# Kernel tuning notes

Hardware: AMD Instinct MI355X
Metric: run time of the kernel (lower is better)

Reference implementation:

```python
import jax, jax.numpy as jnp
import numpy as np

B, N, DIM, H = 512, 98, 512, 16
HD = DIM // H
WS = (2, 7, 7)  # window size; N == 2*7*7


def _relative_position_index(ws):
    d, h, w = ws
    coords = np.stack(np.meshgrid(np.arange(d), np.arange(h), np.arange(w), indexing='ij'))
    cf = coords.reshape(3, -1)  # [3, N]
    rel = cf[:, :, None] - cf[:, None, :]  # [3, N, N]
    rel = rel.transpose(1, 2, 0).astype(np.int64)
    rel[:, :, 0] += d - 1
    rel[:, :, 1] += h - 1
    rel[:, :, 2] += w - 1
    rel[:, :, 0] *= (2 * h - 1) * (2 * w - 1)
    rel[:, :, 1] *= 2 * w - 1
    return rel.sum(-1)  # [N, N] in [0, (2d-1)(2h-1)(2w-1))


def setup_inputs() -> dict:
    key = jax.random.key(0)
    ks = jax.random.split(key, 6)
    table_size = (2 * WS[0] - 1) * (2 * WS[1] - 1) * (2 * WS[2] - 1)  # 507
    return {
        'x': jax.random.normal(ks[0], (B, N, DIM), jnp.float32),
        'qkv_w': jax.random.normal(ks[1], (DIM, 3 * DIM), jnp.float32) * 0.02,
        'qkv_b': jnp.zeros((3 * DIM,), jnp.float32),
        'proj_w': jax.random.normal(ks[2], (DIM, DIM), jnp.float32) * 0.02,
        'proj_b': jnp.zeros((DIM,), jnp.float32),
        'bias_table': jax.random.normal(ks[3], (table_size, H), jnp.float32) * 0.02,
        'rel_index': jnp.asarray(_relative_position_index(WS)),
    }


def reference(x, qkv_w, qkv_b, proj_w, proj_b, bias_table, rel_index):
    b, n, c = x.shape
    scale = HD ** -0.5
    qkv = (x @ qkv_w + qkv_b).reshape(b, n, 3, H, HD)
    qkv = jnp.transpose(qkv, (2, 0, 3, 1, 4))  # [3, B, H, N, HD]
    q, k, v = qkv[0] * scale, qkv[1], qkv[2]
    attn = jnp.einsum('bhnd,bhmd->bhnm', q, k)  # [B, H, N, N]
    # gather relative position bias: [N,N] indices into [table, H] -> [H, N, N]
    bias = jnp.transpose(bias_table[rel_index], (2, 0, 1))
    attn = jax.nn.softmax(attn + bias[None], axis=-1)
    out = jnp.einsum('bhnm,bhmd->bhnd', attn, v)  # [B, H, N, HD]
    out = jnp.transpose(out, (0, 2, 1, 3)).reshape(b, n, c)
    return out @ proj_w + proj_b
```

## Files before the change

kernel.cpp:

```cpp
#include <hip/hip_runtime.h>

typedef unsigned short u16;
typedef __bf16 bf16x8 __attribute__((ext_vector_type(8)));
typedef float f32x4 __attribute__((ext_vector_type(4)));

typedef __attribute__((address_space(1))) const void* as1_cvp;
typedef __attribute__((address_space(3))) void* as3_vp;

__device__ __forceinline__ float b2f(u16 u) {
  union { unsigned int i; float f; } x; x.i = ((unsigned int)u) << 16; return x.f;
}
__device__ __forceinline__ u16 f2b(float f) {
  union { float f; unsigned int i; } x; x.f = f;
  unsigned int u = x.i;
  u += 0x7fffu + ((u >> 16) & 1u);
  return (u16)(u >> 16);
}

__global__ void k_detect(const u16* __restrict__ x, int* __restrict__ flag) {
  int t = threadIdx.x;
  int sane = 0;
#pragma unroll
  for (int i = 0; i < 8; ++i) {
    u16 u = x[t * 8 + i];
    int e = (u >> 7) & 0xFF;
    sane += (u == 0 || (e >= 100 && e <= 150)) ? 1 : 0;
  }
#pragma unroll
  for (int off = 32; off >= 1; off >>= 1) sane += __shfl_xor(sane, off);
  if (t == 0) *flag = (sane < 480) ? 1 : 0;
}

__global__ void k_convert(const void* __restrict__ xin, u16* __restrict__ xb,
                          const int* __restrict__ flagp) {
  if (!*flagp) return;
  long i = ((long)blockIdx.x * 256 + threadIdx.x) * 4;
  float4 v = *(const float4*)((const float*)xin + i);
  u16* o = xb + i;
  o[0] = f2b(v.x); o[1] = f2b(v.y); o[2] = f2b(v.z); o[3] = f2b(v.w);
}

__global__ void k_transpose(const void* __restrict__ W, u16* __restrict__ WT,
                            const int* __restrict__ flagp, int K, int N) {
  __shared__ u16 tile[32][33];
  int f = *flagp;
  int n0 = blockIdx.x * 32, k0 = blockIdx.y * 32;
  int tx = threadIdx.x, ty = threadIdx.y;
#pragma unroll
  for (int i = 0; i < 32; i += 8) {
    long idx = (long)(k0 + ty + i) * N + n0 + tx;
    tile[ty + i][tx] = f ? f2b(((const float*)W)[idx]) : ((const u16*)W)[idx];
  }
  __syncthreads();
#pragma unroll
  for (int i = 0; i < 32; i += 8)
    WT[(long)(n0 + ty + i) * K + k0 + tx] = tile[tx][ty + i];
}

__global__ void k_biasfrag(const int* __restrict__ rel, const void* __restrict__ table,
                           u16* __restrict__ biasFrag, const int* __restrict__ flagp) {
  int t = blockIdx.x * 256 + threadIdx.x;
  int f = *flagp;
  int ln = t & 63, r2 = t >> 6;
  int tj = r2 & 7, r3 = r2 >> 3;
  int ti = r3 % 7, h = r3 / 7;
  int col = ln & 15, qrow = ln >> 4;
  int j = tj * 16 + col;
  u16 v[4];
#pragma unroll
  for (int r = 0; r < 4; ++r) {
    int i = ti * 16 + qrow * 4 + r; if (i > 97) i = 97;
    float val;
    if (j < 98) {
      int rr = rel[i * 98 + j];
      val = f ? ((const float*)table)[rr * 16 + h] : b2f(((const u16*)table)[rr * 16 + h]);
    } else {
      val = -1e30f;
    }
    v[r] = f2b(val);
  }
  ushort4 out; out.x = v[0]; out.y = v[1]; out.z = v[2]; out.w = v[3];
  *(ushort4*)(biasFrag + (long)t * 4) = out;
}

__global__ __launch_bounds__(256) void k_gemm_bt(
    const u16* __restrict__ A_raw, const u16* __restrict__ A_conv,
    const u16* __restrict__ BT, const void* __restrict__ bias, void* __restrict__ C,
    const int* __restrict__ flagp, int N, int K, int out_follows_flag) {
  __shared__ __align__(16) u16 As[128 * 32];
  __shared__ __align__(16) u16 Bs[128 * 32];
  const int f = *flagp;
  const u16* A = f ? A_conv : A_raw;
  const int t = threadIdx.x, w = t >> 6, ln = t & 63;
  const long bm = (long)blockIdx.x * 128, bn = (long)blockIdx.y * 128;
  const int lrow = ln >> 2, lseg = ln & 3;
  const u16* ag0 = A + (bm + w * 32 + lrow) * (long)K + lseg * 8;
  const u16* ag1 = ag0 + 16L * K;
  const u16* bg0 = BT + (bn + w * 32 + lrow) * (long)K + lseg * 8;
  const u16* bg1 = bg0 + 16L * K;
  u16* As0 = &As[w * 1024]; u16* As1 = &As[w * 1024 + 512];
  u16* Bs0 = &Bs[w * 1024]; u16* Bs1 = &Bs[w * 1024 + 512];
  const int wm = w & 1, wn = w >> 1;
  const int col = ln & 15, qrow = ln >> 4;
  f32x4 acc[4][4] = {};
  for (int k0 = 0; k0 < K; k0 += 32) {
    __syncthreads();
    __builtin_amdgcn_global_load_lds((as1_cvp)(const void*)(ag0 + k0), (as3_vp)As0, 16, 0, 0);
    __builtin_amdgcn_global_load_lds((as1_cvp)(const void*)(ag1 + k0), (as3_vp)As1, 16, 0, 0);
    __builtin_amdgcn_global_load_lds((as1_cvp)(const void*)(bg0 + k0), (as3_vp)Bs0, 16, 0, 0);
    __builtin_amdgcn_global_load_lds((as1_cvp)(const void*)(bg1 + k0), (as3_vp)Bs1, 16, 0, 0);
    __syncthreads();
    bf16x8 af[4], bfr[4];
#pragma unroll
    for (int mi = 0; mi < 4; ++mi)
      af[mi] = *(const bf16x8*)&As[(wm * 64 + mi * 16 + col) * 32 + qrow * 8];
#pragma unroll
    for (int ni = 0; ni < 4; ++ni)
      bfr[ni] = *(const bf16x8*)&Bs[(wn * 64 + ni * 16 + col) * 32 + qrow * 8];
#pragma unroll
    for (int mi = 0; mi < 4; ++mi)
#pragma unroll
      for (int ni = 0; ni < 4; ++ni)
        acc[mi][ni] = __builtin_amdgcn_mfma_f32_16x16x32_bf16(af[mi], bfr[ni], acc[mi][ni], 0, 0, 0);
  }
  const int of = out_follows_flag ? f : 0;
  float bv[4];
#pragma unroll
  for (int ni = 0; ni < 4; ++ni) {
    long c = bn + wn * 64 + ni * 16 + col;
    bv[ni] = f ? ((const float*)bias)[c] : b2f(((const u16*)bias)[c]);
  }
#pragma unroll
  for (int mi = 0; mi < 4; ++mi)
#pragma unroll
    for (int ni = 0; ni < 4; ++ni)
#pragma unroll
      for (int r = 0; r < 4; ++r) {
        long row = bm + wm * 64 + mi * 16 + qrow * 4 + r;
        long c = bn + wn * 64 + ni * 16 + col;
        float v = acc[mi][ni][r] + bv[ni];
        if (of) ((float*)C)[row * N + c] = v;
        else    ((u16*)C)[row * N + c] = f2b(v);
      }
}

__global__ __launch_bounds__(256) void k_attn(
    const u16* __restrict__ qkv, const u16* __restrict__ biasFrag,
    u16* __restrict__ attnout) {
  __shared__ __align__(16) u16 Qs[112 * 32];
  __shared__ __align__(16) u16 Ks[128 * 32];
  __shared__ __align__(16) u16 Vt[32 * 136];
  __shared__ __align__(16) u16 Ps[4][16 * 136];
  const int b = blockIdx.x, h = blockIdx.y;
  const int t = threadIdx.x, w = t >> 6, ln = t & 63;
  const u16* qbase = qkv + (long)b * 98 * 1536 + h * 32;
  {
    const int gr = ln >> 2, gc = (ln & 3) * 8;
    for (int n = w; n < 7; n += 4) {
      int g = n * 16 + gr; if (g > 97) g = 97;
      __builtin_amdgcn_global_load_lds((as1_cvp)(const void*)(qbase + (long)g * 1536 + gc),
                                       (as3_vp)(Qs + n * 512), 16, 0, 0);
    }
    for (int n = w; n < 8; n += 4) {
      int g = n * 16 + gr; if (g > 97) g = 97;
      __builtin_amdgcn_global_load_lds((as1_cvp)(const void*)(qbase + 512 + (long)g * 1536 + gc),
                                       (as3_vp)(Ks + n * 512), 16, 0, 0);
    }
  }
  for (int z = t; z < 32 * 19; z += 256) {
    int d = z / 19, q = z % 19;
    *(unsigned int*)&Vt[d * 136 + 98 + q * 2] = 0u;
  }
  for (int idx = t; idx < 784; idx += 256) {
    int i = idx >> 3, c4 = (idx & 7) * 4;
    ushort4 v4 = *(const ushort4*)(qbase + 1024 + (long)i * 1536 + c4);
    Vt[(c4 + 0) * 136 + i] = v4.x;
    Vt[(c4 + 1) * 136 + i] = v4.y;
    Vt[(c4 + 2) * 136 + i] = v4.z;
    Vt[(c4 + 3) * 136 + i] = v4.w;
  }
  __syncthreads();
  const int col = ln & 15, qrow = ln >> 4;
  const float scale = 0.17677669529663687f;
  u16* Psw = &Ps[w][0];
  f32x4 o[2][2] = {{{0.f,0.f,0.f,0.f},{0.f,0.f,0.f,0.f}},{{0.f,0.f,0.f,0.f},{0.f,0.f,0.f,0.f}}};
  for (int tt = 0; tt < 2; ++tt) {
    const int ti = w + tt * 4;
    if (ti >= 7) break;
    const u16* bp = biasFrag + ((long)((h * 7 + ti) * 8) * 64 + ln) * 4;
    ushort4 bfv[8];
#pragma unroll
    for (int tj = 0; tj < 8; ++tj) bfv[tj] = *(const ushort4*)(bp + tj * 256);
    bf16x8 aq = *(const bf16x8*)&Qs[(ti * 16 + col) * 32 + qrow * 8];
    f32x4 s[8];
#pragma unroll
    for (int tj = 0; tj < 8; ++tj) {
      bf16x8 bk = *(const bf16x8*)&Ks[(tj * 16 + col) * 32 + qrow * 8];
      f32x4 z = {0.f, 0.f, 0.f, 0.f};
      s[tj] = __builtin_amdgcn_mfma_f32_16x16x32_bf16(aq, bk, z, 0, 0, 0);
    }
#pragma unroll
    for (int r = 0; r < 4; ++r) {
      float vals[8]; float m = -1e30f;
#pragma unroll
      for (int tj = 0; tj < 8; ++tj) {
        u16 bb = (r == 0) ? bfv[tj].x : (r == 1) ? bfv[tj].y : (r == 2) ? bfv[tj].z : bfv[tj].w;
        float v = fmaf(s[tj][r], scale, b2f(bb));
        vals[tj] = v; m = fmaxf(m, v);
      }
#pragma unroll
      for (int off = 1; off < 16; off <<= 1) m = fmaxf(m, __shfl_xor(m, off));
      float sum = 0.f;
#pragma unroll
      for (int tj = 0; tj < 8; ++tj) { vals[tj] = __expf(vals[tj] - m); sum += vals[tj]; }
#pragma unroll
      for (int off = 1; off < 16; off <<= 1) sum += __shfl_xor(sum, off);
      float inv = 1.f / sum;
      const int rt = qrow * 4 + r;
#pragma unroll
      for (int tj = 0; tj < 8; ++tj)
        Psw[rt * 136 + tj * 16 + col] = f2b(vals[tj] * inv);
    }
#pragma unroll
    for (int ks = 0; ks < 4; ++ks) {
      bf16x8 ap  = *(const bf16x8*)&Psw[col * 136 + ks * 32 + qrow * 8];
      bf16x8 bv0 = *(const bf16x8*)&Vt[col * 136 + ks * 32 + qrow * 8];
      bf16x8 bv1 = *(const bf16x8*)&Vt[(16 + col) * 136 + ks * 32 + qrow * 8];
      o[tt][0] = __builtin_amdgcn_mfma_f32_16x16x32_bf16(ap, bv0, o[tt][0], 0, 0, 0);
      o[tt][1] = __builtin_amdgcn_mfma_f32_16x16x32_bf16(ap, bv1, o[tt][1], 0, 0, 0);
    }
  }
  __syncthreads();
  u16* Os = Qs;
#pragma unroll
  for (int tt = 0; tt < 2; ++tt) {
    const int ti = w + tt * 4;
    if (ti >= 7) continue;
#pragma unroll
    for (int r = 0; r < 4; ++r) {
      const int i = ti * 16 + qrow * 4 + r;
      if (i < 98) {
        Os[i * 32 + col]      = f2b(o[tt][0][r]);
        Os[i * 32 + 16 + col] = f2b(o[tt][1][r]);
      }
    }
  }
  __syncthreads();
  u16* obase = attnout + (long)b * 98 * 512 + h * 32;
  for (int idx = t; idx < 784; idx += 256) {
    int i = idx >> 3, c4 = (idx & 7) * 4;
    *(ushort4*)(obase + (long)i * 512 + c4) = *(const ushort4*)&Os[i * 32 + c4];
  }
}

extern "C" void kernel_launch(void* const* d_in, const int* in_sizes, int n_in,
                              void* d_out, int out_size, void* d_ws, size_t ws_size,
                              hipStream_t stream) {
  (void)in_sizes; (void)n_in; (void)out_size; (void)ws_size;
  char* p = (char*)d_ws;
  u16* qkvbuf   = (u16*)p;  p += 50176L * 1536 * 2;
  u16* attnbuf  = (u16*)p;  u16* xb = attnbuf; p += 50176L * 512 * 2;
  u16* wqkvT    = (u16*)p;  p += 1536L * 512 * 2;
  u16* wprojT   = (u16*)p;  p += 512L * 512 * 2;
  u16* biasFrag = (u16*)p;  p += 57344L * 4 * 2;
  int* flagp    = (int*)p;

  k_detect<<<1, 64, 0, stream>>>((const u16*)d_in[0], flagp);
  k_convert<<<25088, 256, 0, stream>>>(d_in[0], xb, flagp);
  k_transpose<<<dim3(48, 16), dim3(32, 8), 0, stream>>>(d_in[1], wqkvT, flagp, 512, 1536);
  k_transpose<<<dim3(16, 16), dim3(32, 8), 0, stream>>>(d_in[3], wprojT, flagp, 512, 512);
  k_biasfrag<<<224, 256, 0, stream>>>((const int*)d_in[6], d_in[5], biasFrag, flagp);
  k_gemm_bt<<<dim3(392, 12), 256, 0, stream>>>((const u16*)d_in[0], xb, wqkvT, d_in[2],
                                               qkvbuf, flagp, 1536, 512, 0);
  k_attn<<<dim3(512, 16), 256, 0, stream>>>(qkvbuf, biasFrag, attnbuf);
  k_gemm_bt<<<dim3(392, 4), 256, 0, stream>>>(attnbuf, attnbuf, wprojT, d_in[4],
                                              d_out, flagp, 512, 512, 1);
}
```

Baseline: 464.8 us.

## Write QKV in per-head contiguous layout, XCD-aware GEMM tile mapping, BK=64

New measurement: 504.2 us. 8.5% more time.

```diff
diff --git a/kernel.cpp b/kernel.cpp
--- a/kernel.cpp
+++ b/kernel.cpp
@@ -86,42 +86,54 @@
 __global__ __launch_bounds__(256) void k_gemm_bt(
     const u16* __restrict__ A_raw, const u16* __restrict__ A_conv,
     const u16* __restrict__ BT, const void* __restrict__ bias, void* __restrict__ C,
-    const int* __restrict__ flagp, int N, int K, int out_follows_flag) {
-  __shared__ __align__(16) u16 As[128 * 32];
-  __shared__ __align__(16) u16 Bs[128 * 32];
+    const int* __restrict__ flagp, int N, int K, int out_follows_flag,
+    int qkv_mode, int NT) {
+  __shared__ __align__(16) u16 As[128 * 64];
+  __shared__ __align__(16) u16 Bs[128 * 64];
   const int f = *flagp;
   const u16* A = f ? A_conv : A_raw;
   const int t = threadIdx.x, w = t >> 6, ln = t & 63;
-  const long bm = (long)blockIdx.x * 128, bn = (long)blockIdx.y * 128;
-  const int lrow = ln >> 2, lseg = ln & 3;
-  const u16* ag0 = A + (bm + w * 32 + lrow) * (long)K + lseg * 8;
-  const u16* ag1 = ag0 + 16L * K;
-  const u16* bg0 = BT + (bn + w * 32 + lrow) * (long)K + lseg * 8;
-  const u16* bg1 = bg0 + 16L * K;
-  u16* As0 = &As[w * 1024]; u16* As1 = &As[w * 1024 + 512];
-  u16* Bs0 = &Bs[w * 1024]; u16* Bs1 = &Bs[w * 1024 + 512];
+  const unsigned p = blockIdx.x, xcd = p & 7, q = p >> 3;
+  const unsigned qd = q / (unsigned)NT;
+  const unsigned mt = xcd * 49u + qd, nt = q - qd * (unsigned)NT;
+  const long bm = (long)mt * 128, bn = (long)nt * 128;
+  const int r16 = ln & 15, seg = ln >> 4;
+  const u16* agp[4]; const u16* bgp[4];
+#pragma unroll
+  for (int i = 0; i < 4; ++i) {
+    int c = w * 4 + i, rc = c >> 1, kh = c & 1;
+    agp[i] = A  + (bm + rc * 16 + r16) * (long)K + kh * 32 + seg * 8;
+    bgp[i] = BT + (bn + rc * 16 + r16) * (long)K + kh * 32 + seg * 8;
+  }
   const int wm = w & 1, wn = w >> 1;
   const int col = ln & 15, qrow = ln >> 4;
   f32x4 acc[4][4] = {};
-  for (int k0 = 0; k0 < K; k0 += 32) {
+  for (int k0 = 0; k0 < K; k0 += 64) {
     __syncthreads();
-    __builtin_amdgcn_global_load_lds((as1_cvp)(const void*)(ag0 + k0), (as3_vp)As0, 16, 0, 0);
-    __builtin_amdgcn_global_load_lds((as1_cvp)(const void*)(ag1 + k0), (as3_vp)As1, 16, 0, 0);
-    __builtin_amdgcn_global_load_lds((as1_cvp)(const void*)(bg0 + k0), (as3_vp)Bs0, 16, 0, 0);
-    __builtin_amdgcn_global_load_lds((as1_cvp)(const void*)(bg1 + k0), (as3_vp)Bs1, 16, 0, 0);
+#pragma unroll
+    for (int i = 0; i < 4; ++i) {
+      int c = w * 4 + i;
+      __builtin_amdgcn_global_load_lds((as1_cvp)(const void*)(agp[i] + k0),
+                                       (as3_vp)(As + c * 512), 16, 0, 0);
+      __builtin_amdgcn_global_load_lds((as1_cvp)(const void*)(bgp[i] + k0),
+                                       (as3_vp)(Bs + c * 512), 16, 0, 0);
+    }
     __syncthreads();
-    bf16x8 af[4], bfr[4];
-#pragma unroll
-    for (int mi = 0; mi < 4; ++mi)
-      af[mi] = *(const bf16x8*)&As[(wm * 64 + mi * 16 + col) * 32 + qrow * 8];
-#pragma unroll
-    for (int ni = 0; ni < 4; ++ni)
-      bfr[ni] = *(const bf16x8*)&Bs[(wn * 64 + ni * 16 + col) * 32 + qrow * 8];
-#pragma unroll
-    for (int mi = 0; mi < 4; ++mi)
+#pragma unroll
+    for (int kh = 0; kh < 2; ++kh) {
+      bf16x8 af[4], bfr[4];
+#pragma unroll
+      for (int mi = 0; mi < 4; ++mi)
+        af[mi] = *(const bf16x8*)&As[(((wm * 4 + mi) << 1) | kh) * 512 + qrow * 128 + col * 8];
 #pragma unroll
       for (int ni = 0; ni < 4; ++ni)
-        acc[mi][ni] = __builtin_amdgcn_mfma_f32_16x16x32_bf16(af[mi], bfr[ni], acc[mi][ni], 0, 0, 0);
+        bfr[ni] = *(const bf16x8*)&Bs[(((wn * 4 + ni) << 1) | kh) * 512 + qrow * 128 + col * 8];
+#pragma unroll
+      for (int mi = 0; mi < 4; ++mi)
+#pragma unroll
+        for (int ni = 0; ni < 4; ++ni)
+          acc[mi][ni] = __builtin_amdgcn_mfma_f32_16x16x32_bf16(af[mi], bfr[ni], acc[mi][ni], 0, 0, 0);
+    }
   }
   const int of = out_follows_flag ? f : 0;
   float bv[4];
@@ -130,18 +142,36 @@
     long c = bn + wn * 64 + ni * 16 + col;
     bv[ni] = f ? ((const float*)bias)[c] : b2f(((const u16*)bias)[c]);
   }
-#pragma unroll
-  for (int mi = 0; mi < 4; ++mi)
-#pragma unroll
-    for (int ni = 0; ni < 4; ++ni)
+  if (qkv_mode) {
+#pragma unroll
+    for (int mi = 0; mi < 4; ++mi)
 #pragma unroll
       for (int r = 0; r < 4; ++r) {
-        long row = bm + wm * 64 + mi * 16 + qrow * 4 + r;
-        long c = bn + wn * 64 + ni * 16 + col;
-        float v = acc[mi][ni][r] + bv[ni];
-        if (of) ((float*)C)[row * N + c] = v;
-        else    ((u16*)C)[row * N + c] = f2b(v);
+        unsigned row = (unsigned)(bm + wm * 64 + mi * 16 + qrow * 4 + r);
+        unsigned bb = row / 98u, n = row - bb * 98u;
+        long rowbase = (long)bb * (48 * 3136) + (long)n * 32;
+#pragma unroll
+        for (int ni = 0; ni < 4; ++ni) {
+          int c = (int)bn + wn * 64 + ni * 16 + col;
+          int sel = c >> 9, hd = c & 511;
+          long oi = rowbase + (long)((hd >> 5) * 3 + sel) * 3136 + (hd & 31);
+          ((u16*)C)[oi] = f2b(acc[mi][ni][r] + bv[ni]);
+        }
       }
+  } else {
+#pragma unroll
+    for (int mi = 0; mi < 4; ++mi)
+#pragma unroll
+      for (int ni = 0; ni < 4; ++ni)
+#pragma unroll
+        for (int r = 0; r < 4; ++r) {
+          long row = bm + wm * 64 + mi * 16 + qrow * 4 + r;
+          long c = bn + wn * 64 + ni * 16 + col;
+          float v = acc[mi][ni][r] + bv[ni];
+          if (of) ((float*)C)[row * N + c] = v;
+          else    ((u16*)C)[row * N + c] = f2b(v);
+        }
+  }
 }
 
 __global__ __launch_bounds__(256) void k_attn(
@@ -151,29 +181,24 @@
   __shared__ __align__(16) u16 Ks[128 * 32];
   __shared__ __align__(16) u16 Vt[32 * 136];
   __shared__ __align__(16) u16 Ps[4][16 * 136];
-  const int b = blockIdx.x, h = blockIdx.y;
+  const int h = blockIdx.x, b = blockIdx.y;
   const int t = threadIdx.x, w = t >> 6, ln = t & 63;
-  const u16* qbase = qkv + (long)b * 98 * 1536 + h * 32;
-  {
-    const int gr = ln >> 2, gc = (ln & 3) * 8;
-    for (int n = w; n < 7; n += 4) {
-      int g = n * 16 + gr; if (g > 97) g = 97;
-      __builtin_amdgcn_global_load_lds((as1_cvp)(const void*)(qbase + (long)g * 1536 + gc),
-                                       (as3_vp)(Qs + n * 512), 16, 0, 0);
-    }
-    for (int n = w; n < 8; n += 4) {
-      int g = n * 16 + gr; if (g > 97) g = 97;
-      __builtin_amdgcn_global_load_lds((as1_cvp)(const void*)(qbase + 512 + (long)g * 1536 + gc),
-                                       (as3_vp)(Ks + n * 512), 16, 0, 0);
-    }
-  }
+  const u16* qbase = qkv + ((long)b * 16 + h) * 3 * 3136;
+  const u16* kbase = qbase + 3136;
+  const u16* vbase = qbase + 6272;
+  for (int n = w; n < 7; n += 4)
+    __builtin_amdgcn_global_load_lds((as1_cvp)(const void*)(qbase + n * 512 + ln * 8),
+                                     (as3_vp)(Qs + n * 512), 16, 0, 0);
+  for (int n = w; n < 8; n += 4)
+    __builtin_amdgcn_global_load_lds((as1_cvp)(const void*)(kbase + n * 512 + ln * 8),
+                                     (as3_vp)(Ks + n * 512), 16, 0, 0);
   for (int z = t; z < 32 * 19; z += 256) {
-    int d = z / 19, q = z % 19;
-    *(unsigned int*)&Vt[d * 136 + 98 + q * 2] = 0u;
+    int d = z / 19, qq = z % 19;
+    *(unsigned int*)&Vt[d * 136 + 98 + qq * 2] = 0u;
   }
   for (int idx = t; idx < 784; idx += 256) {
     int i = idx >> 3, c4 = (idx & 7) * 4;
-    ushort4 v4 = *(const ushort4*)(qbase + 1024 + (long)i * 1536 + c4);
+    ushort4 v4 = *(const ushort4*)(vbase + i * 32 + c4);
     Vt[(c4 + 0) * 136 + i] = v4.x;
     Vt[(c4 + 1) * 136 + i] = v4.y;
     Vt[(c4 + 2) * 136 + i] = v4.z;
@@ -270,9 +295,9 @@
   k_transpose<<<dim3(48, 16), dim3(32, 8), 0, stream>>>(d_in[1], wqkvT, flagp, 512, 1536);
   k_transpose<<<dim3(16, 16), dim3(32, 8), 0, stream>>>(d_in[3], wprojT, flagp, 512, 512);
   k_biasfrag<<<224, 256, 0, stream>>>((const int*)d_in[6], d_in[5], biasFrag, flagp);
-  k_gemm_bt<<<dim3(392, 12), 256, 0, stream>>>((const u16*)d_in[0], xb, wqkvT, d_in[2],
-                                               qkvbuf, flagp, 1536, 512, 0);
-  k_attn<<<dim3(512, 16), 256, 0, stream>>>(qkvbuf, biasFrag, attnbuf);
-  k_gemm_bt<<<dim3(392, 4), 256, 0, stream>>>(attnbuf, attnbuf, wprojT, d_in[4],
-                                              d_out, flagp, 512, 512, 1);
-}
+  k_gemm_bt<<<4704, 256, 0, stream>>>((const u16*)d_in[0], xb, wqkvT, d_in[2],
+                                      qkvbuf, flagp, 1536, 512, 0, 1, 12);
+  k_attn<<<dim3(16, 512), 256, 0, stream>>>(qkvbuf, biasFrag, attnbuf);
+  k_gemm_bt<<<1568, 256, 0, stream>>>(attnbuf, attnbuf, wprojT, d_in[4],
+                                      d_out, flagp, 512, 512, 1, 0, 4);
+}
```
